# Performance work log

Hardware: AMD Instinct MI355X
Metric: run time of the kernel (lower is better)

The kernel has to match this reference:

```python
import jax, jax.numpy as jnp
jax.config.update("jax_enable_x64", True)
import numpy as np

LEAF = 0.3          # leaf_voxel_size
FACTOR = 2.0        # scale_up_factor
LEVELS = 3          # voxel_level_num
DIM = 8             # feature_dim
BUF = 5000000       # hash_buffer_size
NFEAT = 4194304     # entries per level feature table
PRIMES = jnp.array([73856093, 19349669, 83492791], dtype=jnp.int64)
STEPS = jnp.array([[0.,0.,0.],[0.,0.,1.],[0.,1.,0.],[0.,1.,1.],
                   [1.,0.,0.],[1.,0.,1.],[1.,1.,0.],[1.,1.,1.]], dtype=jnp.float32)

def setup_inputs() -> dict:
    key = jax.random.key(0)
    k1, k2, k3 = jax.random.split(key, 3)
    query_points = jax.random.normal(k1, (1000000, 3), dtype=jnp.float32) * 25.0
    features = 0.01 * jax.random.normal(k2, (LEVELS, NFEAT, DIM), dtype=jnp.float32)
    index_table = jax.random.randint(k3, (LEVELS, BUF), 0, NFEAT, dtype=jnp.int64)
    return {"query_points": query_points, "features": features, "index_table": index_table}

def _level_features(points, feats, idx_table, res):
    # points: [N,3], feats: [F,D], idx_table: [BUF] int64
    base = jnp.floor(points / res)                       # [N,3]
    corners = base[:, None, :] + STEPS[None]             # [N,8,3]
    keys = (corners.astype(jnp.int64) * PRIMES).sum(-1) % BUF  # [N,8]
    idx = idx_table[keys]                                # [N,8]
    mask = idx.min(axis=1) > -1                          # point valid iff all 8 corners mapped
    gathered = feats[jnp.maximum(idx, 0)]                # [N,8,D]
    d = points / res - base                              # fractional coords in cell, [N,3]
    # trilinear weights, corner order matches STEPS (same as torch interpolat)
    w = (STEPS[None] * d[:, None, :] + (1.0 - STEPS[None]) * (1.0 - d[:, None, :])).prod(-1)  # [N,8]
    lvl = (gathered * w[..., None]).sum(1)               # [N,D]
    return jnp.where(mask[:, None], lvl, 0.0)

def reference(query_points, features, index_table):
    out = jnp.zeros((query_points.shape[0], DIM), dtype=jnp.float32)
    for i in range(LEVELS):
        res = LEAF * FACTOR ** i
        out = out + _level_features(query_points, features[i], index_table[i], res)
    return out
```

## Files before the change

### kernel.cpp

```cpp
#include <hip/hip_runtime.h>


constexpr int       BUF   = 5000000;
constexpr long long NFEAT = 4194304;
constexpr int       DIM   = 8;
constexpr long long P0 = 73856093, P1 = 19349669, P2 = 83492791;

typedef float vf4 __attribute__((ext_vector_type(4)));

__global__ __launch_bounds__(256, 4) void nvh_kernel(
    const float* __restrict__ qp,
    const float* __restrict__ feats,
    const int* __restrict__ idx_tab,
    float* __restrict__ out, int n)
{
    int i = blockIdx.x * blockDim.x + threadIdx.x;
    if (i >= n) return;

    const float px = qp[3 * i + 0];
    const float py = qp[3 * i + 1];
    const float pz = qp[3 * i + 2];

    const float resv[3] = {0.3f, 0.6f, 1.2f};

    float dxv[3], dyv[3], dzv[3];
    int idxv[3][8];
#pragma unroll
    for (int lvl = 0; lvl < 3; ++lvl) {
        const float res = resv[lvl];
        const float fx = px / res, fy = py / res, fz = pz / res;
        const float bx = floorf(fx), by = floorf(fy), bz = floorf(fz);
        dxv[lvl] = fx - bx; dyv[lvl] = fy - by; dzv[lvl] = fz - bz;

        const long long ix = (long long)bx;
        const long long iy = (long long)by;
        const long long iz = (long long)bz;

        long long h0 = (ix * P0 + iy * P1 + iz * P2) % (long long)BUF;
        if (h0 < 0) h0 += BUF;
        const int k0 = (int)h0;

        const int* tab = idx_tab + (size_t)lvl * BUF;
#pragma unroll
        for (int c = 0; c < 8; ++c) {
            const long long offc = (((c >> 2) & 1) * P0 + ((c >> 1) & 1) * P1 +
                                    (c & 1) * P2) % (long long)BUF;
            int k = k0 + (int)offc;
            if (k >= BUF) k -= BUF;
            idxv[lvl][c] = tab[k];
        }
    }
    __builtin_amdgcn_sched_barrier(0);

    vf4 acc0 = (vf4)0.0f;
    vf4 acc1 = (vf4)0.0f;

#pragma unroll
    for (int lvl = 0; lvl < 3; ++lvl) {
        const float* fb = feats + (size_t)lvl * (size_t)NFEAT * DIM;

        bool valid = true;
        unsigned off[8];
#pragma unroll
        for (int c = 0; c < 8; ++c) {
            valid = valid && (idxv[lvl][c] > -1);
            const int id = idxv[lvl][c] > 0 ? idxv[lvl][c] : 0;
            off[c] = (unsigned)id * (unsigned)DIM;
        }

        vf4 f[16];
#pragma unroll
        for (int c = 0; c < 8; ++c) {
            const vf4* fp = (const vf4*)(fb + off[c]);
            f[2 * c + 0] = __builtin_nontemporal_load(fp + 0);
            f[2 * c + 1] = __builtin_nontemporal_load(fp + 1);
        }
        __builtin_amdgcn_sched_barrier(0);

        const float dx = dxv[lvl], dy = dyv[lvl], dz = dzv[lvl];
        const float wx1 = dx, wx0 = 1.0f - dx;
        const float wy1 = dy, wy0 = 1.0f - dy;
        const float wz1 = dz, wz0 = 1.0f - dz;

        vf4 lacc0 = (vf4)0.0f;
        vf4 lacc1 = (vf4)0.0f;
#pragma unroll
        for (int c = 0; c < 8; ++c) {
            const float wc = (((c >> 2) & 1) ? wx1 : wx0) *
                             (((c >> 1) & 1) ? wy1 : wy0) *
                             (((c     ) & 1) ? wz1 : wz0);
            lacc0 += wc * f[2 * c + 0];
            lacc1 += wc * f[2 * c + 1];
        }

        if (valid) { acc0 += lacc0; acc1 += lacc1; }
    }

    vf4* op = (vf4*)(out + (size_t)i * DIM);
    __builtin_nontemporal_store(acc0, op + 0);
    __builtin_nontemporal_store(acc1, op + 1);
}

extern "C" void kernel_launch(void* const* d_in, const int* in_sizes, int n_in,
                              void* d_out, int out_size, void* d_ws, size_t ws_size,
                              hipStream_t stream) {
    const float* qp      = (const float*)d_in[0];
    const float* feats   = (const float*)d_in[1];
    const int*   idx_tab = (const int*)d_in[2];
    float*       out     = (float*)d_out;

    const int n = in_sizes[0] / 3;
    const int block = 256;
    const int grid = (n + block - 1) / block;
    hipLaunchKernelGGL(nvh_kernel, dim3(grid), dim3(block), 0, stream,
                       qp, feats, idx_tab, out, n);
}
```

Measured before the change: 1.334 ms.

## Software-pipeline feature gathers across levels with inline asm loads and manual waitcnt

Replaces the per-level gather-then-math loop with a pipelined schedule. Gathers for levels 0 and 1 are issued together. Level 2's gathers are issued after level 0's math. Explicit s_waitcnt vmcnt counters let math overlap with outstanding loads. Loads become inline asm global_load_dwordx4 with SGPR base plus VGPR offset. The validity branch becomes a multiply by a 0/1 mask. Launch bounds drop from 4 to 3 waves per SIMD to make room for the extra live registers, which lowers occupancy and risks a worse balance for this latency-bound gather. The hand-written waitcnt values must match the asm load count, and the compiler does not track them.

```diff
diff --git a/kernel.cpp b/kernel.cpp
--- a/kernel.cpp
+++ b/kernel.cpp
@@ -8,7 +8,14 @@
 
 typedef float vf4 __attribute__((ext_vector_type(4)));
 
-__global__ __launch_bounds__(256, 4) void nvh_kernel(
+#define GLD_NT0(dst, voff, base)                                   \
+    asm volatile("global_load_dwordx4 %0, %1, %2 nt"               \
+                 : "=v"(dst) : "v"(voff), "s"(base))
+#define GLD_NT16(dst, voff, base)                                  \
+    asm volatile("global_load_dwordx4 %0, %1, %2 offset:16 nt"     \
+                 : "=v"(dst) : "v"(voff), "s"(base))
+
+__global__ __launch_bounds__(256, 3) void nvh_kernel(
     const float* __restrict__ qp,
     const float* __restrict__ feats,
     const int* __restrict__ idx_tab,
@@ -52,49 +59,79 @@
     }
     __builtin_amdgcn_sched_barrier(0);
 
-    vf4 acc0 = (vf4)0.0f;
-    vf4 acc1 = (vf4)0.0f;
-
+    unsigned voff[3][8];
+    float vm[3];
 #pragma unroll
     for (int lvl = 0; lvl < 3; ++lvl) {
-        const float* fb = feats + (size_t)lvl * (size_t)NFEAT * DIM;
-
         bool valid = true;
-        unsigned off[8];
 #pragma unroll
         for (int c = 0; c < 8; ++c) {
             valid = valid && (idxv[lvl][c] > -1);
             const int id = idxv[lvl][c] > 0 ? idxv[lvl][c] : 0;
-            off[c] = (unsigned)id * (unsigned)DIM;
+            voff[lvl][c] = (unsigned)id * 32u;
         }
+        vm[lvl] = valid ? 1.0f : 0.0f;
+    }
 
-        vf4 f[16];
+    const float* fb0 = feats;
+    const float* fb1 = feats + (size_t)1 * (size_t)NFEAT * DIM;
+    const float* fb2 = feats + (size_t)2 * (size_t)NFEAT * DIM;
+
+    vf4 f0[16], f1[16], f2[16];
+
 #pragma unroll
-        for (int c = 0; c < 8; ++c) {
-            const vf4* fp = (const vf4*)(fb + off[c]);
-            f[2 * c + 0] = __builtin_nontemporal_load(fp + 0);
-            f[2 * c + 1] = __builtin_nontemporal_load(fp + 1);
-        }
-        __builtin_amdgcn_sched_barrier(0);
+    for (int c = 0; c < 8; ++c) {
+        GLD_NT0 (f0[2 * c + 0], voff[0][c], fb0);
+        GLD_NT16(f0[2 * c + 1], voff[0][c], fb0);
+    }
+#pragma unroll
+    for (int c = 0; c < 8; ++c) {
+        GLD_NT0 (f1[2 * c + 0], voff[1][c], fb1);
+        GLD_NT16(f1[2 * c + 1], voff[1][c], fb1);
+    }
 
-        const float dx = dxv[lvl], dy = dyv[lvl], dz = dzv[lvl];
-        const float wx1 = dx, wx0 = 1.0f - dx;
-        const float wy1 = dy, wy0 = 1.0f - dy;
-        const float wz1 = dz, wz0 = 1.0f - dz;
+    vf4 acc0 = (vf4)0.0f;
+    vf4 acc1 = (vf4)0.0f;
 
-        vf4 lacc0 = (vf4)0.0f;
-        vf4 lacc1 = (vf4)0.0f;
+#define LEVEL_MATH(F, LVL)                                                  \
+    do {                                                                    \
+        const float dx = dxv[LVL], dy = dyv[LVL], dz = dzv[LVL];            \
+        const float wx1 = dx, wx0 = 1.0f - dx;                              \
+        const float wy1 = dy, wy0 = 1.0f - dy;                              \
+        const float wz1 = dz, wz0 = 1.0f - dz;                              \
+        vf4 lacc0 = (vf4)0.0f;                                              \
+        vf4 lacc1 = (vf4)0.0f;                                              \
+        _Pragma("unroll")                                                   \
+        for (int c = 0; c < 8; ++c) {                                       \
+            const float wc = (((c >> 2) & 1) ? wx1 : wx0) *                 \
+                             (((c >> 1) & 1) ? wy1 : wy0) *                 \
+                             (((c     ) & 1) ? wz1 : wz0);                  \
+            lacc0 += wc * F[2 * c + 0];                                     \
+            lacc1 += wc * F[2 * c + 1];                                     \
+        }                                                                   \
+        acc0 += vm[LVL] * lacc0;                                            \
+        acc1 += vm[LVL] * lacc1;                                            \
+    } while (0)
+
+    asm volatile("s_waitcnt vmcnt(16)" ::: "memory");
+    __builtin_amdgcn_sched_barrier(0);
+    LEVEL_MATH(f0, 0);
+
 #pragma unroll
-        for (int c = 0; c < 8; ++c) {
-            const float wc = (((c >> 2) & 1) ? wx1 : wx0) *
-                             (((c >> 1) & 1) ? wy1 : wy0) *
-                             (((c     ) & 1) ? wz1 : wz0);
-            lacc0 += wc * f[2 * c + 0];
-            lacc1 += wc * f[2 * c + 1];
-        }
+    for (int c = 0; c < 8; ++c) {
+        GLD_NT0 (f2[2 * c + 0], voff[2][c], fb2);
+        GLD_NT16(f2[2 * c + 1], voff[2][c], fb2);
+    }
 
-        if (valid) { acc0 += lacc0; acc1 += lacc1; }
-    }
+    asm volatile("s_waitcnt vmcnt(16)" ::: "memory");
+    __builtin_amdgcn_sched_barrier(0);
+    LEVEL_MATH(f1, 1);
+
+    asm volatile("s_waitcnt vmcnt(0)" ::: "memory");
+    __builtin_amdgcn_sched_barrier(0);
+    LEVEL_MATH(f2, 2);
+
+#undef LEVEL_MATH
 
     vf4* op = (vf4*)(out + (size_t)i * DIM);
     __builtin_nontemporal_store(acc0, op + 0);
```

Measured after the change: 1.323 ms. Within noise of the previous version (-0.8%).

## Split fused three-level kernel into per-level launches accumulating into output

Applied to the files above, without the earlier changes.

Replaces the single kernel that processes all three hash levels per point with three launches, one per level, each reading and adding into the output buffer. This keeps each launch's working set to one level's index and feature table (about 128 MB plus 20 MB), which may improve cache locality of the random gathers. The feature loads become inline-asm global_load_dwordx4 with a scalar base and an explicit vmcnt wait, and validity is applied as a multiplicative mask. In exchange it re-reads the query points and does extra output read/write traffic across launches, and drops the nontemporal hints.

```diff
diff --git a/kernel.cpp b/kernel.cpp
--- a/kernel.cpp
+++ b/kernel.cpp
@@ -8,11 +8,19 @@
 
 typedef float vf4 __attribute__((ext_vector_type(4)));
 
-__global__ __launch_bounds__(256, 4) void nvh_kernel(
+#define GLD0(dst, voff, base)                                  \
+    asm volatile("global_load_dwordx4 %0, %1, %2"              \
+                 : "=v"(dst) : "v"(voff), "s"(base))
+#define GLD16(dst, voff, base)                                 \
+    asm volatile("global_load_dwordx4 %0, %1, %2 offset:16"    \
+                 : "=v"(dst) : "v"(voff), "s"(base))
+
+template <bool ADD>
+__global__ __launch_bounds__(256, 4) void nvh_level_kernel(
     const float* __restrict__ qp,
-    const float* __restrict__ feats,
-    const int* __restrict__ idx_tab,
-    float* __restrict__ out, int n)
+    const float* __restrict__ fb,
+    const int* __restrict__ tab,
+    float* __restrict__ out, int n, float res)
 {
     int i = blockIdx.x * blockDim.x + threadIdx.x;
     if (i >= n) return;
@@ -21,84 +29,78 @@
     const float py = qp[3 * i + 1];
     const float pz = qp[3 * i + 2];
 
-    const float resv[3] = {0.3f, 0.6f, 1.2f};
+    const float fx = px / res, fy = py / res, fz = pz / res;
+    const float bx = floorf(fx), by = floorf(fy), bz = floorf(fz);
+    const float dx = fx - bx, dy = fy - by, dz = fz - bz;
 
-    float dxv[3], dyv[3], dzv[3];
-    int idxv[3][8];
+    const long long ix = (long long)bx;
+    const long long iy = (long long)by;
+    const long long iz = (long long)bz;
+
+    long long h0 = (ix * P0 + iy * P1 + iz * P2) % (long long)BUF;
+    if (h0 < 0) h0 += BUF;
+    const int k0 = (int)h0;
+
+    int idxv[8];
 #pragma unroll
-    for (int lvl = 0; lvl < 3; ++lvl) {
-        const float res = resv[lvl];
-        const float fx = px / res, fy = py / res, fz = pz / res;
-        const float bx = floorf(fx), by = floorf(fy), bz = floorf(fz);
-        dxv[lvl] = fx - bx; dyv[lvl] = fy - by; dzv[lvl] = fz - bz;
-
-        const long long ix = (long long)bx;
-        const long long iy = (long long)by;
-        const long long iz = (long long)bz;
-
-        long long h0 = (ix * P0 + iy * P1 + iz * P2) % (long long)BUF;
-        if (h0 < 0) h0 += BUF;
-        const int k0 = (int)h0;
-
-        const int* tab = idx_tab + (size_t)lvl * BUF;
-#pragma unroll
-        for (int c = 0; c < 8; ++c) {
-            const long long offc = (((c >> 2) & 1) * P0 + ((c >> 1) & 1) * P1 +
-                                    (c & 1) * P2) % (long long)BUF;
-            int k = k0 + (int)offc;
-            if (k >= BUF) k -= BUF;
-            idxv[lvl][c] = tab[k];
-        }
+    for (int c = 0; c < 8; ++c) {
+        const long long offc = (((c >> 2) & 1) * P0 + ((c >> 1) & 1) * P1 +
+                                (c & 1) * P2) % (long long)BUF;
+        int k = k0 + (int)offc;
+        if (k >= BUF) k -= BUF;
+        idxv[c] = tab[k];
     }
     __builtin_amdgcn_sched_barrier(0);
 
-    vf4 acc0 = (vf4)0.0f;
-    vf4 acc1 = (vf4)0.0f;
-
+    bool valid = true;
+    unsigned voff[8];
 #pragma unroll
-    for (int lvl = 0; lvl < 3; ++lvl) {
-        const float* fb = feats + (size_t)lvl * (size_t)NFEAT * DIM;
-
-        bool valid = true;
-        unsigned off[8];
-#pragma unroll
-        for (int c = 0; c < 8; ++c) {
-            valid = valid && (idxv[lvl][c] > -1);
-            const int id = idxv[lvl][c] > 0 ? idxv[lvl][c] : 0;
-            off[c] = (unsigned)id * (unsigned)DIM;
-        }
-
-        vf4 f[16];
-#pragma unroll
-        for (int c = 0; c < 8; ++c) {
-            const vf4* fp = (const vf4*)(fb + off[c]);
-            f[2 * c + 0] = __builtin_nontemporal_load(fp + 0);
-            f[2 * c + 1] = __builtin_nontemporal_load(fp + 1);
-        }
-        __builtin_amdgcn_sched_barrier(0);
-
-        const float dx = dxv[lvl], dy = dyv[lvl], dz = dzv[lvl];
-        const float wx1 = dx, wx0 = 1.0f - dx;
-        const float wy1 = dy, wy0 = 1.0f - dy;
-        const float wz1 = dz, wz0 = 1.0f - dz;
-
-        vf4 lacc0 = (vf4)0.0f;
-        vf4 lacc1 = (vf4)0.0f;
-#pragma unroll
-        for (int c = 0; c < 8; ++c) {
-            const float wc = (((c >> 2) & 1) ? wx1 : wx0) *
-                             (((c >> 1) & 1) ? wy1 : wy0) *
-                             (((c     ) & 1) ? wz1 : wz0);
-            lacc0 += wc * f[2 * c + 0];
-            lacc1 += wc * f[2 * c + 1];
-        }
-
-        if (valid) { acc0 += lacc0; acc1 += lacc1; }
+    for (int c = 0; c < 8; ++c) {
+        valid = valid && (idxv[c] > -1);
+        const int id = idxv[c] > 0 ? idxv[c] : 0;
+        voff[c] = (unsigned)id * 32u;
     }
 
+    vf4 f[16];
+#pragma unroll
+    for (int c = 0; c < 8; ++c) {
+        GLD0 (f[2 * c + 0], voff[c], fb);
+        GLD16(f[2 * c + 1], voff[c], fb);
+    }
+
+    vf4 prev0, prev1;
+    if (ADD) {
+        const vf4* op = (const vf4*)(out + (size_t)i * DIM);
+        prev0 = op[0];
+        prev1 = op[1];
+    }
+
+    const float wx1 = dx, wx0 = 1.0f - dx;
+    const float wy1 = dy, wy0 = 1.0f - dy;
+    const float wz1 = dz, wz0 = 1.0f - dz;
+    const float vmask = valid ? 1.0f : 0.0f;
+
+    asm volatile("s_waitcnt vmcnt(0)" ::: "memory");
+    __builtin_amdgcn_sched_barrier(0);
+
+    vf4 lacc0 = (vf4)0.0f;
+    vf4 lacc1 = (vf4)0.0f;
+#pragma unroll
+    for (int c = 0; c < 8; ++c) {
+        const float wc = (((c >> 2) & 1) ? wx1 : wx0) *
+                         (((c >> 1) & 1) ? wy1 : wy0) *
+                         (((c     ) & 1) ? wz1 : wz0);
+        lacc0 += wc * f[2 * c + 0];
+        lacc1 += wc * f[2 * c + 1];
+    }
+
+    vf4 r0 = vmask * lacc0;
+    vf4 r1 = vmask * lacc1;
+    if (ADD) { r0 += prev0; r1 += prev1; }
+
     vf4* op = (vf4*)(out + (size_t)i * DIM);
-    __builtin_nontemporal_store(acc0, op + 0);
-    __builtin_nontemporal_store(acc1, op + 1);
+    op[0] = r0;
+    op[1] = r1;
 }
 
 extern "C" void kernel_launch(void* const* d_in, const int* in_sizes, int n_in,
@@ -112,6 +114,13 @@
     const int n = in_sizes[0] / 3;
     const int block = 256;
     const int grid = (n + block - 1) / block;
-    hipLaunchKernelGGL(nvh_kernel, dim3(grid), dim3(block), 0, stream,
-                       qp, feats, idx_tab, out, n);
+
+    hipLaunchKernelGGL((nvh_level_kernel<false>), dim3(grid), dim3(block), 0,
+                       stream, qp, feats, idx_tab, out, n, 0.3f);
+    hipLaunchKernelGGL((nvh_level_kernel<true>), dim3(grid), dim3(block), 0,
+                       stream, qp, feats + (size_t)1 * NFEAT * DIM,
+                       idx_tab + (size_t)1 * BUF, out, n, 0.6f);
+    hipLaunchKernelGGL((nvh_level_kernel<true>), dim3(grid), dim3(block), 0,
+                       stream, qp, feats + (size_t)2 * NFEAT * DIM,
+                       idx_tab + (size_t)2 * BUF, out, n, 1.2f);
 }
```

New measurement: 1.258 ms. 5.7% less time.
